# Optimization experiments

Hardware: AMD Instinct MI355X
Metric: run time of the kernel (lower is better)

The kernel has to match this reference:

```python
import jax, jax.numpy as jnp
import numpy as np

NUM_SPLIT = 4

def setup_inputs() -> dict:
    key = jax.random.key(0)
    x = jax.random.normal(key, (8, 64, 256, 256), dtype=jnp.float32)
    return {"x": x}

def reference(x) -> jnp.ndarray:
    # x: [B, S*cell^2, H, W] with H == W. Per split group, channel index p within
    # a group maps to intra-block (row, col) = (p // cell, p % cell); block (h, w)
    # of the output is the cell x cell patch from spatial position (h, w).
    B, C, H, W = x.shape
    S = NUM_SPLIT
    cpg = C // S                      # channels per group = cell^2
    cell = int(round(np.sqrt(cpg)))
    # [B, S, cell_r, cell_c, H, W] -> [B, S, H, cell_r, W, cell_c] -> [B, S, H*cell, W*cell]
    out = x.reshape(B, S, cell, cell, H, W)
    out = out.transpose(0, 1, 4, 2, 5, 3)
    return out.reshape(B, S, H * cell, W * cell)
```

## Files before the change

kernel.cpp:

```cpp
#include <hip/hip_runtime.h>


#define TOTAL_ELEMS (8 * 64 * 256 * 256)
#define TOTAL_F4    (TOTAL_ELEMS / 4)
#define CH_STRIDE   65536

__global__ __launch_bounds__(256) void DepthToSpace_8486855377460_kernel(
    const float* __restrict__ in, float* __restrict__ out) {
    int idx4 = blockIdx.x * blockDim.x + threadIdx.x;
    int base = idx4 << 2;

    int ww = base & 1023;
    int hh = (base >> 10) & 1023;
    int s  = (base >> 20) & 3;
    int b  = base >> 22;

    int w = ww >> 2;
    int r = hh & 3;
    int h = hh >> 2;
    int c = (s << 4) + (r << 2);

    int in_off = (((b << 6) + c) << 16) + (h << 8) + w;

    float4 v;
    v.x = in[in_off];
    v.y = in[in_off + 1 * CH_STRIDE];
    v.z = in[in_off + 2 * CH_STRIDE];
    v.w = in[in_off + 3 * CH_STRIDE];

    reinterpret_cast<float4*>(out)[idx4] = v;
}

extern "C" void kernel_launch(void* const* d_in, const int* in_sizes, int n_in,
                              void* d_out, int out_size, void* d_ws, size_t ws_size,
                              hipStream_t stream) {
    const float* x = (const float*)d_in[0];
    float* out = (float*)d_out;
    dim3 block(256);
    dim3 grid(TOTAL_F4 / 256);
    DepthToSpace_8486855377460_kernel<<<grid, block, 0, stream>>>(x, out);
}
```

Before: 223.4 us.

## Stage depth-to-space tile through LDS for vectorized reads and writes

Each block now handles one (batch, split, row) tile. It loads 16 channel rows with float4 global reads into shared memory, synchronizes, then assembles float4 outputs from LDS and writes 4 contiguous output rows. This replaces the scalar strided global loads with fully vectorized coalesced loads, at the cost of 16KB of LDS per block and a barrier.

```diff
diff --git a/kernel.cpp b/kernel.cpp
--- a/kernel.cpp
+++ b/kernel.cpp
@@ -1,34 +1,41 @@
 #include <hip/hip_runtime.h>
 
 
-#define TOTAL_ELEMS (8 * 64 * 256 * 256)
-#define TOTAL_F4    (TOTAL_ELEMS / 4)
-#define CH_STRIDE   65536
+#define CH_STRIDE 65536
 
 __global__ __launch_bounds__(256) void DepthToSpace_8486855377460_kernel(
     const float* __restrict__ in, float* __restrict__ out) {
-    int idx4 = blockIdx.x * blockDim.x + threadIdx.x;
-    int base = idx4 << 2;
+    __shared__ float lds[16 * 256];
 
-    int ww = base & 1023;
-    int hh = (base >> 10) & 1023;
-    int s  = (base >> 20) & 3;
-    int b  = base >> 22;
+    int t = threadIdx.x;
+    int idx = blockIdx.x;
+    int h = idx & 255;
+    int s = (idx >> 8) & 3;
+    int b = idx >> 10;
 
-    int w = ww >> 2;
-    int r = hh & 3;
-    int h = hh >> 2;
-    int c = (s << 4) + (r << 2);
+    const float* src = in + ((size_t)(b * 64 + s * 16)) * CH_STRIDE + h * 256;
 
-    int in_off = (((b << 6) + c) << 16) + (h << 8) + w;
+#pragma unroll
+    for (int k = 0; k < 4; ++k) {
+        int j = k * 256 + t;
+        int ch = j >> 6;
+        int w4 = j & 63;
+        float4 v = *(const float4*)(src + ch * CH_STRIDE + w4 * 4);
+        *(float4*)(&lds[ch * 256 + w4 * 4]) = v;
+    }
 
-    float4 v;
-    v.x = in[in_off];
-    v.y = in[in_off + 1 * CH_STRIDE];
-    v.z = in[in_off + 2 * CH_STRIDE];
-    v.w = in[in_off + 3 * CH_STRIDE];
+    __syncthreads();
 
-    reinterpret_cast<float4*>(out)[idx4] = v;
+    float* dst = out + (((size_t)(b * 4 + s) * 1024) + h * 4) * 1024;
+#pragma unroll
+    for (int r = 0; r < 4; ++r) {
+        float4 v;
+        v.x = lds[(4 * r + 0) * 256 + t];
+        v.y = lds[(4 * r + 1) * 256 + t];
+        v.z = lds[(4 * r + 2) * 256 + t];
+        v.w = lds[(4 * r + 3) * 256 + t];
+        ((float4*)(dst + r * 1024))[t] = v;
+    }
 }
 
 extern "C" void kernel_launch(void* const* d_in, const int* in_sizes, int n_in,
@@ -37,6 +44,6 @@
     const float* x = (const float*)d_in[0];
     float* out = (float*)d_out;
     dim3 block(256);
-    dim3 grid(TOTAL_F4 / 256);
+    dim3 grid(8 * 4 * 256);
     DepthToSpace_8486855377460_kernel<<<grid, block, 0, stream>>>(x, out);
 }
```

Result: no change. 226.7 us (+1.4%).
